# Kernel optimization log

Hardware: AMD Instinct MI355X
Metric: run time of the kernel (lower is better)

The kernel has to match this reference:

```python
import jax, jax.numpy as jnp
import numpy as np

N, NFEAT, NHID, NREL, NCLASS, NHEADS = 4096, 512, 64, 64, 16, 8
ALPHA = 0.2   # LeakyReLU negative slope
NEG = -9e15   # pyGAT mask value


def _gat_layer(x, rel, mask, adj_ad, W, a1, a2, concat):
    # x: [N, Fin], rel: [nrel, Fin], mask: [N, N] bool, adj_ad: [N, nrel]
    xr = x + adj_ad @ rel                 # relation-augmented node features
    h = xr @ W                            # [N, Fout]
    f1 = h @ a1                           # [N]  (a^T[Wh_i||Wh_j] = f1_i + f2_j)
    f2 = h @ a2                           # [N]
    e = jax.nn.leaky_relu(f1[:, None] + f2[None, :], ALPHA)  # [N, N]
    att = jax.nn.softmax(jnp.where(mask, e, NEG), axis=1)
    out = att @ h                         # [N, Fout]
    return jax.nn.elu(out) if concat else out


def setup_inputs() -> dict:
    key = jax.random.key(0)
    ks = jax.random.split(key, 12)
    x = jax.random.normal(ks[0], (N, NFEAT), jnp.float32)
    rel = jax.random.normal(ks[1], (NREL, NFEAT), jnp.float32)
    rel_dict = jax.random.randint(ks[2], (N,), 0, NREL, jnp.int32)
    adj = (jax.random.uniform(ks[3], (N, N)) < 0.01).astype(jnp.float32)
    adj = jnp.maximum(adj, jnp.eye(N, dtype=jnp.float32))  # self loops
    adj_ad = jax.random.uniform(ks[4], (N, NREL), jnp.float32)
    adj_ad = adj_ad / adj_ad.sum(axis=1, keepdims=True)
    s_in = 1.0 / np.sqrt(NFEAT)
    s_hid = 1.0 / np.sqrt(NHID)
    s_cat = 1.0 / np.sqrt(NHID * NHEADS)
    W_heads = jax.random.normal(ks[5], (NHEADS, NFEAT, NHID), jnp.float32) * s_in
    a1_heads = jax.random.normal(ks[6], (NHEADS, NHID), jnp.float32) * s_hid
    a2_heads = jax.random.normal(ks[7], (NHEADS, NHID), jnp.float32) * s_hid
    W_out = jax.random.normal(ks[8], (NHID * NHEADS, NFEAT), jnp.float32) * s_cat
    a1_out = jax.random.normal(ks[9], (NFEAT,), jnp.float32) * s_in
    a2_out = jax.random.normal(ks[10], (NFEAT,), jnp.float32) * s_in
    lin_W = jax.random.normal(ks[11], (NFEAT, NCLASS), jnp.float32) * s_in
    lin_b = jnp.zeros((NCLASS,), jnp.float32)
    return {"x": x, "rel": rel, "rel_dict": rel_dict, "adj": adj, "adj_ad": adj_ad,
            "W_heads": W_heads, "a1_heads": a1_heads, "a2_heads": a2_heads,
            "W_out": W_out, "a1_out": a1_out, "a2_out": a2_out,
            "lin_W": lin_W, "lin_b": lin_b}


def reference(x, rel, rel_dict, adj, adj_ad, W_heads, a1_heads, a2_heads,
              W_out, a1_out, a2_out, lin_W, lin_b):
    # dropout is identity at inference (training=False); rel_dict is only used
    # by the repo to build adj/adj_ad, so it is a non-math constant here.
    mask = adj > 0
    # multi-head GAT layer, heads fused via vmap then concatenated on feature dim
    heads = jax.vmap(lambda W, a1, a2: _gat_layer(x, rel, mask, adj_ad, W, a1, a2, True))(
        W_heads, a1_heads, a2_heads)                      # [H, N, NHID]
    hcat = jnp.moveaxis(heads, 0, 1).reshape(N, NHEADS * NHID)  # [N, H*NHID]
    h2 = _gat_layer(hcat, rel, mask, adj_ad, W_out, a1_out, a2_out, False)  # [N, NFEAT]
    logits = jax.nn.elu(h2 @ lin_W + lin_b)               # [N, NCLASS]
    return jax.nn.log_softmax(logits, axis=1)
```

## Files before the change

### kernel.cpp

```cpp
#include <hip/hip_runtime.h>

#define NN      4096
#define FEAT    512
#define NHID    64
#define NHEADS  8
#define NCLS    16
#define MAXDEG  128
#define ALPHA   0.2f

typedef __bf16 bf16_t;
typedef __bf16 bf16x8_t __attribute__((ext_vector_type(8)));
typedef float  f32x4_t  __attribute__((ext_vector_type(4)));
typedef unsigned short us8_t __attribute__((ext_vector_type(8)));

__device__ inline unsigned short f2bf(float f) {
    unsigned int u = __float_as_uint(f);
    u += 0x7fffu + ((u >> 16) & 1u);
    return (unsigned short)(u >> 16);
}
__device__ inline float bfu2f(unsigned short b) {
    return __uint_as_float(((unsigned int)b) << 16);
}

__global__ __launch_bounds__(128) void rmmfuse_kernel(
    const float* __restrict__ adj_ad, const float* __restrict__ rel,
    const float* __restrict__ x, float* __restrict__ R,
    bf16_t* __restrict__ Abf) {
    int i = blockIdx.x;
    int t = threadIdx.x;
    __shared__ float sa[64];
    if (t < 64) sa[t] = adj_ad[i * 64 + t];
    __syncthreads();
    float4 acc = make_float4(0.f, 0.f, 0.f, 0.f);
    for (int r = 0; r < 64; ++r) {
        float a = sa[r];
        float4 rv = ((const float4*)(rel + r * FEAT))[t];
        acc.x += a * rv.x; acc.y += a * rv.y;
        acc.z += a * rv.z; acc.w += a * rv.w;
    }
    ((float4*)(R + (size_t)i * FEAT))[t] = acc;
    float4 xv = ((const float4*)(x + (size_t)i * FEAT))[t];
    ushort4 o;
    o.x = f2bf(acc.x + xv.x); o.y = f2bf(acc.y + xv.y);
    o.z = f2bf(acc.z + xv.z); o.w = f2bf(acc.w + xv.w);
    *(ushort4*)(Abf + (size_t)i * FEAT + 4 * t) = o;
}

__global__ __launch_bounds__(256) void wperm_kernel(
    const float* __restrict__ Wh, const float* __restrict__ Wo,
    unsigned short* __restrict__ WcT, unsigned short* __restrict__ WoT,
    float* __restrict__ f1o, float* __restrict__ f2o) {
    int gid = blockIdx.x * 256 + threadIdx.x;
    if (gid < 262144) {
        int idx = gid;
        int n = idx >> 9, k = idx & 511;
        int h = n >> 6, f = n & 63;
        WcT[idx] = f2bf(Wh[(h * 512 + k) * 64 + f]);
    } else if (gid < 524288) {
        int idx = gid - 262144;
        int n = idx >> 9, k = idx & 511;
        WoT[idx] = f2bf(Wo[k * 512 + n]);
    } else {
        int idx = gid - 524288;
        ((float4*)f1o)[idx] = make_float4(0.f, 0.f, 0.f, 0.f);
        ((float4*)f2o)[idx] = make_float4(0.f, 0.f, 0.f, 0.f);
    }
}

__global__ __launch_bounds__(256) void gemm_bf16_dot_kernel(
    const bf16_t* __restrict__ A, const bf16_t* __restrict__ Bt,
    unsigned short* __restrict__ Cbf,
    const float* __restrict__ a1, const float* __restrict__ a2,
    float* __restrict__ f1, float* __restrict__ f2, int layer2) {
    __shared__ __align__(16) bf16_t As[64][72];
    __shared__ __align__(16) bf16_t Bs[64][72];
    const int bm = blockIdx.x * 64;
    const int bn = blockIdx.y * 64;
    const int t  = threadIdx.x;
    const int lr = t >> 3;
    const int lc = (t & 7) * 8;
    const int l  = t & 63;
    const int w  = t >> 6;
    const int mrow = w * 16 + (l & 15);
    const int nrow = l & 15;
    const int q8 = (l >> 4) * 8;

    f32x4_t acc[4] = {};
    for (int k0 = 0; k0 < FEAT; k0 += 64) {
        *(uint4*)&As[lr][lc]      = *(const uint4*)(A  + (size_t)(bm + lr)      * FEAT + k0 + lc);
        *(uint4*)&As[32 + lr][lc] = *(const uint4*)(A  + (size_t)(bm + 32 + lr) * FEAT + k0 + lc);
        *(uint4*)&Bs[lr][lc]      = *(const uint4*)(Bt + (size_t)(bn + lr)      * FEAT + k0 + lc);
        *(uint4*)&Bs[32 + lr][lc] = *(const uint4*)(Bt + (size_t)(bn + 32 + lr) * FEAT + k0 + lc);
        __syncthreads();
        #pragma unroll
        for (int kk = 0; kk < 64; kk += 32) {
            bf16x8_t a = *(const bf16x8_t*)&As[mrow][kk + q8];
            #pragma unroll
            for (int nt = 0; nt < 4; ++nt) {
                bf16x8_t b = *(const bf16x8_t*)&Bs[nt * 16 + nrow][kk + q8];
                acc[nt] = __builtin_amdgcn_mfma_f32_16x16x32_bf16(a, b, acc[nt], 0, 0, 0);
            }
        }
        __syncthreads();
    }
    const int crow = bm + w * 16 + (l >> 4) * 4;
    const int ccol = bn + (l & 15);
    #pragma unroll
    for (int nt = 0; nt < 4; ++nt)
        #pragma unroll
        for (int r = 0; r < 4; ++r)
            Cbf[(size_t)(crow + r) * FEAT + ccol + nt * 16] = f2bf(acc[nt][r]);

    float a1v[4], a2v[4];
    #pragma unroll
    for (int nt = 0; nt < 4; ++nt) {
        a1v[nt] = a1[bn + (l & 15) + nt * 16];
        a2v[nt] = a2[bn + (l & 15) + nt * 16];
    }
    float p1[4] = {}, p2[4] = {};
    #pragma unroll
    for (int nt = 0; nt < 4; ++nt)
        #pragma unroll
        for (int r = 0; r < 4; ++r) {
            p1[r] += acc[nt][r] * a1v[nt];
            p2[r] += acc[nt][r] * a2v[nt];
        }
    #pragma unroll
    for (int off = 1; off <= 8; off <<= 1)
        #pragma unroll
        for (int r = 0; r < 4; ++r) {
            p1[r] += __shfl_xor(p1[r], off);
            p2[r] += __shfl_xor(p2[r], off);
        }
    if ((l & 15) == 0) {
        int row = bm + w * 16 + (l >> 4) * 4;
        if (layer2) {
            #pragma unroll
            for (int r = 0; r < 4; ++r) {
                atomicAdd(&f1[row + r], p1[r]);
                atomicAdd(&f2[row + r], p2[r]);
            }
        } else {
            #pragma unroll
            for (int r = 0; r < 4; ++r) {
                f1[blockIdx.y * NN + row + r] = p1[r];
                f2[blockIdx.y * NN + row + r] = p2[r];
            }
        }
    }
}

__device__ inline void csr_emit(unsigned long long m, int lane, int* cnt,
                                int* colrow, int j) {
    if (m) {
        int tot = __popcll(m);
        int base = 0;
        if (lane == 0) base = atomicAdd(cnt, tot);
        base = __shfl(base, 0);
        if (m & (1ULL << lane)) {
            int pos = __popcll(m & ((1ULL << lane) - 1));
            int idx = base + pos;
            if (idx < MAXDEG) colrow[idx] = j;
        }
    }
}
__global__ __launch_bounds__(256) void csr_kernel(
    const float* __restrict__ adj, int* __restrict__ deg, int* __restrict__ cols) {
    int i = blockIdx.x;
    int t = threadIdx.x;
    int lane = t & 63;
    __shared__ int cnt;
    if (t == 0) cnt = 0;
    __syncthreads();
    const float4* row4 = (const float4*)(adj + (size_t)i * NN);
    int* colrow = cols + i * MAXDEG;
    for (int j4 = t; j4 < NN / 4; j4 += 256) {
        float4 v = row4[j4];
        int j = j4 * 4;
        csr_emit(__ballot(v.x > 0.0f), lane, &cnt, colrow, j);
        csr_emit(__ballot(v.y > 0.0f), lane, &cnt, colrow, j + 1);
        csr_emit(__ballot(v.z > 0.0f), lane, &cnt, colrow, j + 2);
        csr_emit(__ballot(v.w > 0.0f), lane, &cnt, colrow, j + 3);
    }
    __syncthreads();
    if (t == 0) deg[i] = cnt > MAXDEG ? MAXDEG : cnt;
}

__global__ __launch_bounds__(512) void att1_kernel(
    const bf16_t* __restrict__ Hbf, const float* __restrict__ f1,
    const float* __restrict__ f2, const int* __restrict__ deg,
    const int* __restrict__ cols, const float* __restrict__ R,
    bf16_t* __restrict__ outbf) {
    int i = blockIdx.x;
    int tid = threadIdx.x;
    int h = tid >> 6;
    int l = tid & 63;
    __shared__ int jl[MAXDEG];
    __shared__ float se[NHEADS][MAXDEG];
    __shared__ float part[NHEADS][FEAT];
    __shared__ float sinv[NHEADS];
    __shared__ int sdeg;
    if (tid == 0) sdeg = deg[i];
    __syncthreads();
    int d = sdeg;
    int dpad = (d + 31) & ~31;
    for (int k = tid; k < dpad; k += 512)
        jl[k] = (k < d) ? cols[i * MAXDEG + k] : i;
    __syncthreads();
    float fi = f1[h * NN + i];
    float lmax = -1e30f;
    for (int k = l; k < d; k += 64) {
        float e = fi + f2[h * NN + jl[k]];
        e = e > 0.0f ? e : ALPHA * e;
        se[h][k] = e;
        lmax = fmaxf(lmax, e);
    }
    for (int off = 32; off; off >>= 1) lmax = fmaxf(lmax, __shfl_down(lmax, off));
    float m = __shfl(lmax, 0);
    float ls = 0.0f;
    for (int k = l; k < d; k += 64) {
        float p = __expf(se[h][k] - m);
        se[h][k] = p;
        ls += p;
    }
    for (int k = d + l; k < dpad; k += 64) se[h][k] = 0.0f;
    for (int off = 32; off; off >>= 1) ls += __shfl_down(ls, off);
    if (l == 0) sinv[h] = 1.0f / ls;
    __syncthreads();
    const int myhead = l >> 3;
    float acc[8] = {};
    for (int k0 = 0; k0 < dpad; k0 += 32) {
        float pw[4];
        const bf16_t* rp[4];
        #pragma unroll
        for (int j = 0; j < 4; ++j) {
            int k = k0 + j * 8 + h;
            pw[j] = se[myhead][k];
            rp[j] = Hbf + (size_t)jl[k] * FEAT + l * 8;
        }
        #pragma unroll
        for (int j = 0; j < 4; ++j) {
            us8_t v = *(const us8_t*)rp[j];
            float p = pw[j];
            #pragma unroll
            for (int q = 0; q < 8; ++q) acc[q] += p * bfu2f(v[q]);
        }
    }
    *(float4*)&part[h][l * 8]     = make_float4(acc[0], acc[1], acc[2], acc[3]);
    *(float4*)&part[h][l * 8 + 4] = make_float4(acc[4], acc[5], acc[6], acc[7]);
    __syncthreads();
    {
        float sum = 0.0f;
        #pragma unroll
        for (int w2 = 0; w2 < NHEADS; ++w2) sum += part[w2][tid];
        float o = sum * sinv[tid >> 6];
        o = o > 0.0f ? o : __expf(o) - 1.0f;
        o += R[(size_t)i * FEAT + tid];
        ((unsigned short*)outbf)[(size_t)i * FEAT + tid] = f2bf(o);
    }
}

__global__ __launch_bounds__(256) void att2_final_kernel(
    const bf16_t* __restrict__ Hbf, const float* __restrict__ f1,
    const float* __restrict__ f2, const int* __restrict__ deg,
    const int* __restrict__ cols, const float* __restrict__ linW,
    const float* __restrict__ linb, float* __restrict__ out) {
    int i = blockIdx.x;
    int t = threadIdx.x;
    __shared__ int jl[MAXDEG];
    __shared__ float sp[MAXDEG];
    __shared__ float red[4];
    __shared__ float part[3][FEAT];
    __shared__ float hrow[FEAT];
    __shared__ float clsred[16][NCLS];
    __shared__ float sl[NCLS];
    __shared__ int sdeg;
    if (t == 0) sdeg = deg[i];
    __syncthreads();
    int d = sdeg;
    int dpad = (d + 15) & ~15;
    if (t < dpad) jl[t] = (t < d) ? cols[i * MAXDEG + t] : i;
    __syncthreads();
    float e = 0.0f, lmax = -1e30f;
    if (t < d) {
        e = f1[i] + f2[jl[t]];
        e = e > 0.0f ? e : ALPHA * e;
        lmax = e;
    }
    for (int off = 32; off; off >>= 1) lmax = fmaxf(lmax, __shfl_down(lmax, off));
    if ((t & 63) == 0) red[t >> 6] = lmax;
    __syncthreads();
    float m = fmaxf(fmaxf(red[0], red[1]), fmaxf(red[2], red[3]));
    float p = 0.0f;
    if (t < d) p = __expf(e - m);
    if (t < dpad) sp[t] = p;
    float ls = p;
    for (int off = 32; off; off >>= 1) ls += __shfl_down(ls, off);
    __syncthreads();
    if ((t & 63) == 0) red[t >> 6] = ls;
    __syncthreads();
    float s = red[0] + red[1] + red[2] + red[3];
    float inv = 1.0f / s;
    const int slot = t >> 6;
    const int cg   = t & 63;
    float acc[8] = {};
    for (int k0 = 0; k0 < dpad; k0 += 16) {
        float pw[4];
        const bf16_t* rp[4];
        #pragma unroll
        for (int j = 0; j < 4; ++j) {
            int k = k0 + j * 4 + slot;
            pw[j] = sp[k];
            rp[j] = Hbf + (size_t)jl[k] * FEAT + cg * 8;
        }
        #pragma unroll
        for (int j = 0; j < 4; ++j) {
            us8_t v = *(const us8_t*)rp[j];
            float pk = pw[j];
            #pragma unroll
            for (int q = 0; q < 8; ++q) acc[q] += pk * bfu2f(v[q]);
        }
    }
    if (slot > 0) {
        float* dst = &part[slot - 1][cg * 8];
        *(float4*)(dst)     = make_float4(acc[0], acc[1], acc[2], acc[3]);
        *(float4*)(dst + 4) = make_float4(acc[4], acc[5], acc[6], acc[7]);
    }
    __syncthreads();
    if (slot == 0) {
        #pragma unroll
        for (int sl2 = 0; sl2 < 3; ++sl2)
            #pragma unroll
            for (int j = 0; j < 8; ++j) acc[j] += part[sl2][cg * 8 + j];
        float* dst = &hrow[cg * 8];
        *(float4*)(dst)     = make_float4(acc[0] * inv, acc[1] * inv, acc[2] * inv, acc[3] * inv);
        *(float4*)(dst + 4) = make_float4(acc[4] * inv, acc[5] * inv, acc[6] * inv, acc[7] * inv);
    }
    __syncthreads();
    {
        int c = t & 15;
        int seg = t >> 4;
        float partial = 0.0f;
        int f0 = seg * 32;
        #pragma unroll 8
        for (int f = f0; f < f0 + 32; ++f) partial += hrow[f] * linW[f * NCLS + c];
        clsred[seg][c] = partial;
    }
    __syncthreads();
    if (t < NCLS) {
        float logit = linb[t];
        #pragma unroll
        for (int seg = 0; seg < 16; ++seg) logit += clsred[seg][t];
        logit = logit > 0.0f ? logit : __expf(logit) - 1.0f;
        sl[t] = logit;
    }
    __syncthreads();
    if (t < NCLS) {
        float mm = sl[0];
        #pragma unroll
        for (int c = 1; c < NCLS; ++c) mm = fmaxf(mm, sl[c]);
        float ssum = 0.0f;
        #pragma unroll
        for (int c = 0; c < NCLS; ++c) ssum += __expf(sl[c] - mm);
        out[i * NCLS + t] = sl[t] - mm - logf(ssum);
    }
}

extern "C" void kernel_launch(void* const* d_in, const int* in_sizes, int n_in,
                              void* d_out, int out_size, void* d_ws, size_t ws_size,
                              hipStream_t stream) {
    const float* x        = (const float*)d_in[0];
    const float* rel      = (const float*)d_in[1];
    const float* adj      = (const float*)d_in[3];
    const float* adj_ad   = (const float*)d_in[4];
    const float* W_heads  = (const float*)d_in[5];
    const float* a1_heads = (const float*)d_in[6];
    const float* a2_heads = (const float*)d_in[7];
    const float* W_out    = (const float*)d_in[8];
    const float* a1_out   = (const float*)d_in[9];
    const float* a2_out   = (const float*)d_in[10];
    const float* lin_W    = (const float*)d_in[11];
    const float* lin_b    = (const float*)d_in[12];
    float* out = (float*)d_out;

    char* ws = (char*)d_ws;
    bf16_t* Abf  = (bf16_t*)(ws);
    bf16_t* Abf2 = (bf16_t*)(ws + (4u  << 20));
    bf16_t* Hbf1 = (bf16_t*)(ws + (8u  << 20));
    bf16_t* Hbf2 = (bf16_t*)(ws + (12u << 20));
    float*  R    = (float*) (ws + (16u << 20));
    bf16_t* WcT  = (bf16_t*)(ws + (24u << 20));
    bf16_t* WoT  = (bf16_t*)(ws + (24u << 20) + (512u << 10));
    float*  f1   = (float*) (ws + (25u << 20));
    float*  f2   = (float*) (ws + (25u << 20) + (128u << 10));
    float*  f1o  = (float*) (ws + (25u << 20) + (256u << 10));
    float*  f2o  = (float*) (ws + (25u << 20) + (272u << 10));
    int*    deg  = (int*)   (ws + (25u << 20) + (288u << 10));
    int*    cols = (int*)   (ws + (26u << 20));

    csr_kernel<<<NN, 256, 0, stream>>>(adj, deg, cols);
    rmmfuse_kernel<<<NN, 128, 0, stream>>>(adj_ad, rel, x, R, Abf);
    wperm_kernel<<<2052, 256, 0, stream>>>(W_heads, W_out,
        (unsigned short*)WcT, (unsigned short*)WoT, f1o, f2o);
    gemm_bf16_dot_kernel<<<dim3(64, 8), 256, 0, stream>>>(
        Abf, WcT, (unsigned short*)Hbf1, a1_heads, a2_heads, f1, f2, 0);
    att1_kernel<<<NN, 512, 0, stream>>>(Hbf1, f1, f2, deg, cols, R, Abf2);
    gemm_bf16_dot_kernel<<<dim3(64, 8), 256, 0, stream>>>(
        Abf2, WoT, (unsigned short*)Hbf2, a1_out, a2_out, f1o, f2o, 1);
    att2_final_kernel<<<NN, 256, 0, stream>>>(Hbf2, f1o, f2o, deg, cols, lin_W, lin_b, out);
}
```

Baseline: 215.9 us.

## Merge preprocessing kernels into one launch and prefetch GEMM tiles into registers

Three independent preprocessing kernels (CSR build from adj, relation mix plus bf16 conversion, weight transpose and zeroing) are merged into a single kernel that dispatches on block index, so one launch replaces three and the independent work can overlap on the GPU. The relation-mix part now packs two rows per 256-thread block. Separately, the bf16 GEMM loads the next K tile into registers while the MFMAs run on the current shared-memory tile, hiding global load latency. This costs more registers and leaves one heterogeneous kernel whose blocks have uneven amounts of work.

```diff
diff --git a/kernel.cpp b/kernel.cpp
--- a/kernel.cpp
+++ b/kernel.cpp
@@ -22,48 +22,83 @@
     return __uint_as_float(((unsigned int)b) << 16);
 }
 
-__global__ __launch_bounds__(128) void rmmfuse_kernel(
+__device__ inline void csr_emit(unsigned long long m, int lane, int* cnt,
+                                int* colrow, int j) {
+    if (m) {
+        int tot = __popcll(m);
+        int base = 0;
+        if (lane == 0) base = atomicAdd(cnt, tot);
+        base = __shfl(base, 0);
+        if (m & (1ULL << lane)) {
+            int pos = __popcll(m & ((1ULL << lane) - 1));
+            int idx = base + pos;
+            if (idx < MAXDEG) colrow[idx] = j;
+        }
+    }
+}
+
+__global__ __launch_bounds__(256) void prep_kernel(
+    const float* __restrict__ adj, int* __restrict__ deg, int* __restrict__ cols,
     const float* __restrict__ adj_ad, const float* __restrict__ rel,
-    const float* __restrict__ x, float* __restrict__ R,
-    bf16_t* __restrict__ Abf) {
-    int i = blockIdx.x;
-    int t = threadIdx.x;
-    __shared__ float sa[64];
-    if (t < 64) sa[t] = adj_ad[i * 64 + t];
-    __syncthreads();
-    float4 acc = make_float4(0.f, 0.f, 0.f, 0.f);
-    for (int r = 0; r < 64; ++r) {
-        float a = sa[r];
-        float4 rv = ((const float4*)(rel + r * FEAT))[t];
-        acc.x += a * rv.x; acc.y += a * rv.y;
-        acc.z += a * rv.z; acc.w += a * rv.w;
-    }
-    ((float4*)(R + (size_t)i * FEAT))[t] = acc;
-    float4 xv = ((const float4*)(x + (size_t)i * FEAT))[t];
-    ushort4 o;
-    o.x = f2bf(acc.x + xv.x); o.y = f2bf(acc.y + xv.y);
-    o.z = f2bf(acc.z + xv.z); o.w = f2bf(acc.w + xv.w);
-    *(ushort4*)(Abf + (size_t)i * FEAT + 4 * t) = o;
-}
-
-__global__ __launch_bounds__(256) void wperm_kernel(
+    const float* __restrict__ x, float* __restrict__ R, bf16_t* __restrict__ Abf,
     const float* __restrict__ Wh, const float* __restrict__ Wo,
     unsigned short* __restrict__ WcT, unsigned short* __restrict__ WoT,
     float* __restrict__ f1o, float* __restrict__ f2o) {
-    int gid = blockIdx.x * 256 + threadIdx.x;
-    if (gid < 262144) {
-        int idx = gid;
-        int n = idx >> 9, k = idx & 511;
-        int h = n >> 6, f = n & 63;
-        WcT[idx] = f2bf(Wh[(h * 512 + k) * 64 + f]);
-    } else if (gid < 524288) {
-        int idx = gid - 262144;
-        int n = idx >> 9, k = idx & 511;
-        WoT[idx] = f2bf(Wo[k * 512 + n]);
+    int b = blockIdx.x;
+    int t = threadIdx.x;
+    __shared__ int cnt;
+    __shared__ float sa[2][64];
+    if (b < NN) {
+        int lane = t & 63;
+        if (t == 0) cnt = 0;
+        __syncthreads();
+        const float4* row4 = (const float4*)(adj + (size_t)b * NN);
+        int* colrow = cols + b * MAXDEG;
+        for (int j4 = t; j4 < NN / 4; j4 += 256) {
+            float4 v = row4[j4];
+            int j = j4 * 4;
+            csr_emit(__ballot(v.x > 0.0f), lane, &cnt, colrow, j);
+            csr_emit(__ballot(v.y > 0.0f), lane, &cnt, colrow, j + 1);
+            csr_emit(__ballot(v.z > 0.0f), lane, &cnt, colrow, j + 2);
+            csr_emit(__ballot(v.w > 0.0f), lane, &cnt, colrow, j + 3);
+        }
+        __syncthreads();
+        if (t == 0) deg[b] = cnt > MAXDEG ? MAXDEG : cnt;
+    } else if (b < NN + 2048) {
+        int half = t >> 7;
+        int tt = t & 127;
+        int i = (b - NN) * 2 + half;
+        if (tt < 64) sa[half][tt] = adj_ad[i * 64 + tt];
+        __syncthreads();
+        float4 acc = make_float4(0.f, 0.f, 0.f, 0.f);
+        for (int r = 0; r < 64; ++r) {
+            float a = sa[half][r];
+            float4 rv = ((const float4*)(rel + r * FEAT))[tt];
+            acc.x += a * rv.x; acc.y += a * rv.y;
+            acc.z += a * rv.z; acc.w += a * rv.w;
+        }
+        ((float4*)(R + (size_t)i * FEAT))[tt] = acc;
+        float4 xv = ((const float4*)(x + (size_t)i * FEAT))[tt];
+        ushort4 o;
+        o.x = f2bf(acc.x + xv.x); o.y = f2bf(acc.y + xv.y);
+        o.z = f2bf(acc.z + xv.z); o.w = f2bf(acc.w + xv.w);
+        *(ushort4*)(Abf + (size_t)i * FEAT + 4 * tt) = o;
     } else {
-        int idx = gid - 524288;
-        ((float4*)f1o)[idx] = make_float4(0.f, 0.f, 0.f, 0.f);
-        ((float4*)f2o)[idx] = make_float4(0.f, 0.f, 0.f, 0.f);
+        int gid = (b - NN - 2048) * 256 + t;
+        if (gid < 262144) {
+            int idx = gid;
+            int n = idx >> 9, k = idx & 511;
+            int h = n >> 6, f = n & 63;
+            WcT[idx] = f2bf(Wh[(h * 512 + k) * 64 + f]);
+        } else if (gid < 524288) {
+            int idx = gid - 262144;
+            int n = idx >> 9, k = idx & 511;
+            WoT[idx] = f2bf(Wo[k * 512 + n]);
+        } else {
+            int idx = gid - 524288;
+            ((float4*)f1o)[idx] = make_float4(0.f, 0.f, 0.f, 0.f);
+            ((float4*)f2o)[idx] = make_float4(0.f, 0.f, 0.f, 0.f);
+        }
     }
 }
 
@@ -85,13 +120,28 @@
     const int nrow = l & 15;
     const int q8 = (l >> 4) * 8;
 
+    const bf16_t* Ap0 = A  + (size_t)(bm + lr)      * FEAT + lc;
+    const bf16_t* Ap1 = A  + (size_t)(bm + 32 + lr) * FEAT + lc;
+    const bf16_t* Bp0 = Bt + (size_t)(bn + lr)      * FEAT + lc;
+    const bf16_t* Bp1 = Bt + (size_t)(bn + 32 + lr) * FEAT + lc;
+    uint4 ra0 = *(const uint4*)(Ap0);
+    uint4 ra1 = *(const uint4*)(Ap1);
+    uint4 rb0 = *(const uint4*)(Bp0);
+    uint4 rb1 = *(const uint4*)(Bp1);
+
     f32x4_t acc[4] = {};
     for (int k0 = 0; k0 < FEAT; k0 += 64) {
-        *(uint4*)&As[lr][lc]      = *(const uint4*)(A  + (size_t)(bm + lr)      * FEAT + k0 + lc);
-        *(uint4*)&As[32 + lr][lc] = *(const uint4*)(A  + (size_t)(bm + 32 + lr) * FEAT + k0 + lc);
-        *(uint4*)&Bs[lr][lc]      = *(const uint4*)(Bt + (size_t)(bn + lr)      * FEAT + k0 + lc);
-        *(uint4*)&Bs[32 + lr][lc] = *(const uint4*)(Bt + (size_t)(bn + 32 + lr) * FEAT + k0 + lc);
+        *(uint4*)&As[lr][lc]      = ra0;
+        *(uint4*)&As[32 + lr][lc] = ra1;
+        *(uint4*)&Bs[lr][lc]      = rb0;
+        *(uint4*)&Bs[32 + lr][lc] = rb1;
         __syncthreads();
+        if (k0 + 64 < FEAT) {
+            ra0 = *(const uint4*)(Ap0 + k0 + 64);
+            ra1 = *(const uint4*)(Ap1 + k0 + 64);
+            rb0 = *(const uint4*)(Bp0 + k0 + 64);
+            rb1 = *(const uint4*)(Bp1 + k0 + 64);
+        }
         #pragma unroll
         for (int kk = 0; kk < 64; kk += 32) {
             bf16x8_t a = *(const bf16x8_t*)&As[mrow][kk + q8];
@@ -148,42 +198,6 @@
             }
         }
     }
-}
-
-__device__ inline void csr_emit(unsigned long long m, int lane, int* cnt,
-                                int* colrow, int j) {
-    if (m) {
-        int tot = __popcll(m);
-        int base = 0;
-        if (lane == 0) base = atomicAdd(cnt, tot);
-        base = __shfl(base, 0);
-        if (m & (1ULL << lane)) {
-            int pos = __popcll(m & ((1ULL << lane) - 1));
-            int idx = base + pos;
-            if (idx < MAXDEG) colrow[idx] = j;
-        }
-    }
-}
-__global__ __launch_bounds__(256) void csr_kernel(
-    const float* __restrict__ adj, int* __restrict__ deg, int* __restrict__ cols) {
-    int i = blockIdx.x;
-    int t = threadIdx.x;
-    int lane = t & 63;
-    __shared__ int cnt;
-    if (t == 0) cnt = 0;
-    __syncthreads();
-    const float4* row4 = (const float4*)(adj + (size_t)i * NN);
-    int* colrow = cols + i * MAXDEG;
-    for (int j4 = t; j4 < NN / 4; j4 += 256) {
-        float4 v = row4[j4];
-        int j = j4 * 4;
-        csr_emit(__ballot(v.x > 0.0f), lane, &cnt, colrow, j);
-        csr_emit(__ballot(v.y > 0.0f), lane, &cnt, colrow, j + 1);
-        csr_emit(__ballot(v.z > 0.0f), lane, &cnt, colrow, j + 2);
-        csr_emit(__ballot(v.w > 0.0f), lane, &cnt, colrow, j + 3);
-    }
-    __syncthreads();
-    if (t == 0) deg[i] = cnt > MAXDEG ? MAXDEG : cnt;
 }
 
 __global__ __launch_bounds__(512) void att1_kernel(
@@ -398,10 +412,9 @@
     int*    deg  = (int*)   (ws + (25u << 20) + (288u << 10));
     int*    cols = (int*)   (ws + (26u << 20));
 
-    csr_kernel<<<NN, 256, 0, stream>>>(adj, deg, cols);
-    rmmfuse_kernel<<<NN, 128, 0, stream>>>(adj_ad, rel, x, R, Abf);
-    wperm_kernel<<<2052, 256, 0, stream>>>(W_heads, W_out,
-        (unsigned short*)WcT, (unsigned short*)WoT, f1o, f2o);
+    prep_kernel<<<NN + 2048 + 2052, 256, 0, stream>>>(
+        adj, deg, cols, adj_ad, rel, x, R, Abf,
+        W_heads, W_out, (unsigned short*)WcT, (unsigned short*)WoT, f1o, f2o);
     gemm_bf16_dot_kernel<<<dim3(64, 8), 256, 0, stream>>>(
         Abf, WcT, (unsigned short*)Hbf1, a1_heads, a2_heads, f1, f2, 0);
     att1_kernel<<<NN, 512, 0, stream>>>(Hbf1, f1, f2, deg, cols, R, Abf2);
```

Measured after the change: 198.7 us. -8.0%, faster.
